# Optimization experiments

Measured on AMD Instinct MI355X. Metric: run time of the kernel, lower is better.

Reference implementation:

```python
import jax, jax.numpy as jnp
import numpy as np

MARGIN = 0.3
NEG_INF = jnp.float32(-1e30)


def setup_inputs() -> dict:
    key = jax.random.key(0)
    k1, k2 = jax.random.split(key)
    features = jax.random.normal(k1, (8192, 128), dtype=jnp.float32)
    labels = jax.random.randint(k2, (8192,), 0, 512)
    return {"features": features, "labels": labels}


def reference(features, labels):
    n = features.shape[0]
    # pairwise Euclidean distance, clamped like the torch code
    x2 = jnp.sum(features * features, axis=1, keepdims=True)          # [N,1]
    d2 = x2 + x2.T - 2.0 * (features @ features.T)                    # [N,N]
    dist = jnp.sqrt(jnp.clip(d2, 1e-8))

    same = labels[None, :] == labels[:, None]                          # [N,N]
    eye = jnp.eye(n, dtype=bool)
    pos_mask = same & ~eye                                             # positives, self excluded
    neg_mask = ~same

    # soft mining: softmax-weighted positive distance (weights ~ softmax(d))
    pos_logits = jnp.where(pos_mask, dist, NEG_INF)
    pw = jax.nn.softmax(pos_logits, axis=1)
    wp = jnp.sum(pw * jnp.where(pos_mask, dist, 0.0), axis=1)          # [N]

    # softmax-weighted negative distance (weights ~ softmax(-d))
    neg_logits = jnp.where(neg_mask, -dist, NEG_INF)
    nw = jax.nn.softmax(neg_logits, axis=1)
    wn = jnp.sum(nw * jnp.where(neg_mask, dist, 0.0), axis=1)          # [N]

    # soft margin: softplus(diff + margin)
    loss = jax.nn.softplus(wp - wn + MARGIN)

    # rows without any positive or any negative are skipped in the original
    valid = pos_mask.any(axis=1) & neg_mask.any(axis=1)
    loss = jnp.where(valid, loss, 0.0)
    denom = jnp.maximum(jnp.sum(valid.astype(jnp.float32)), 1.0)
    return jnp.sum(loss) / denom
```

## Files before the change

### kernel.cpp

```cpp
#include <hip/hip_runtime.h>
#include <hip/hip_bf16.h>


typedef __bf16 bf16x8 __attribute__((ext_vector_type(8)));
typedef float f32x4 __attribute__((ext_vector_type(4)));

#define NROWS 8192
#define DIM 128
#define JTILE 64
#define LDS_STRIDE 136
#define NLABELS 512
#define GCAP 64
#define JSPLIT 16
#define JSPAN (NROWS / JSPLIT)
#define JITERS (JSPAN / JTILE)
#define MARGIN_F 0.3f
#define AK1F 2.04027892f
#define AK1SQ 4.16273807f
#define EPS_T 2.08137e-8f
#define C2F (-43.2808512f)
#define LN2F 0.69314718f

__global__ __launch_bounds__(256) void prep_kernel(const float* __restrict__ F,
                                                   __hip_bfloat16* __restrict__ Fb,
                                                   float* __restrict__ x2,
                                                   float* __restrict__ gstat) {
    const int tid = threadIdx.x;
    const int wave = tid >> 6, lane = tid & 63;
    const int row = blockIdx.x * 4 + wave;
    float2 f = ((const float2*)(F + (size_t)row * DIM))[lane];
    f.x *= AK1F; f.y *= AK1F;
    ((__hip_bfloat162*)(Fb + (size_t)row * DIM))[lane] = __float22bfloat162_rn(f);
    float ss = f.x * f.x + f.y * f.y;
#pragma unroll
    for (int m = 32; m > 0; m >>= 1) ss += __shfl_xor(ss, m, 64);
    if (lane == 0) x2[row] = ss;
    if (blockIdx.x == 0 && tid < 4) gstat[tid] = 0.f;
}

template<bool DIAG>
__device__ __forceinline__ void tile_body(const __hip_bfloat16* __restrict__ sB,
                                          const float* __restrict__ sX2h,
                                          const bf16x8 (&a)[4],
                                          const float (&x2ih)[4],
                                          float (&nl4)[4], float (&ns4)[4],
                                          int lm, int quad, int ig0, int jbase) {
#pragma unroll
    for (int jt = 0; jt < 4; ++jt) {
        const int jl = jt * 16 + lm;
        const __hip_bfloat16* bp = sB + jl * LDS_STRIDE + quad * 8;
        const float xjh = sX2h[jl];
        f32x4 acc;
#pragma unroll
        for (int r = 0; r < 4; ++r) acc[r] = x2ih[r] + xjh;
#pragma unroll
        for (int kc = 0; kc < 4; ++kc) {
            bf16x8 b = *(const bf16x8*)(bp + kc * 32);
            acc = __builtin_amdgcn_mfma_f32_16x16x32_bf16(a[kc], b, acc, 0, 0, 0);
        }
        const int dj = jbase + jl - ig0;
#pragma unroll
        for (int r = 0; r < 4; ++r) {
            float d2h = fmaxf(-acc[r], EPS_T);
            float t = __builtin_amdgcn_sqrtf(d2h);
            float ne = __builtin_amdgcn_exp2f(-t);
            if (DIAG) ne = (dj == r) ? 0.f : ne;
            nl4[r] += ne;
            ns4[r] = fmaf(ne, t, ns4[r]);
        }
    }
}

__global__ __launch_bounds__(256, 4) void pairs_kernel(
        const __hip_bfloat16* __restrict__ Fb,
        const float* __restrict__ x2,
        const float* __restrict__ F,
        const int* __restrict__ labels,
        float2* __restrict__ partial,
        float4* __restrict__ corr) {
    __shared__ __hip_bfloat16 sB[JTILE * LDS_STRIDE];
    __shared__ float sX2[JTILE];
    __shared__ int sIdx[GCAP];
    __shared__ int sCnt;

    const int tid = threadIdx.x;
    const int bx = blockIdx.x, by = blockIdx.y;

    if (by < 4) {
        const int L = by * 128 + bx;
        if (tid == 0) sCnt = 0;
        __syncthreads();
        for (int it = 0; it < NROWS / 1024; ++it) {
            const int g = it * 1024 + tid * 4;
            int4 lv = *(const int4*)(labels + g);
#pragma unroll
            for (int k = 0; k < 4; ++k) {
                int lab = (k == 0) ? lv.x : (k == 1) ? lv.y : (k == 2) ? lv.z : lv.w;
                if (lab == L) {
                    int pos = atomicAdd(&sCnt, 1);
                    if (pos < GCAP) sIdx[pos] = g + k;
                }
            }
        }
        __syncthreads();
        const int gsz = sCnt < GCAP ? sCnt : GCAP;
        if (gsz > 0) {
            float* sAcc = (float*)sB;
            float* plA = sAcc;
            float* psA = sAcc + GCAP;
            float* nlA = sAcc + 2 * GCAP;
            float* nsA = sAcc + 3 * GCAP;
            if (tid < GCAP) { plA[tid] = 0.f; psA[tid] = 0.f; nlA[tid] = 0.f; nsA[tid] = 0.f; }
            __syncthreads();
            const int npair = gsz * gsz;
            for (int p = tid; p < npair; p += 256) {
                const int aI = p / gsz, bI = p - aI * gsz;
                if (aI == bI) continue;
                const float4* pa = (const float4*)(F + (size_t)sIdx[aI] * DIM);
                const float4* pb = (const float4*)(F + (size_t)sIdx[bI] * DIM);
                float dot = 0.f, ssa = 0.f, ssb = 0.f;
#pragma unroll 8
                for (int u = 0; u < 32; ++u) {
                    float4 va = pa[u], vb = pb[u];
                    dot = fmaf(va.x, vb.x, fmaf(va.y, vb.y, fmaf(va.z, vb.z, fmaf(va.w, vb.w, dot))));
                    ssa = fmaf(va.x, va.x, fmaf(va.y, va.y, fmaf(va.z, va.z, fmaf(va.w, va.w, ssa))));
                    ssb = fmaf(vb.x, vb.x, fmaf(vb.y, vb.y, fmaf(vb.z, vb.z, fmaf(vb.w, vb.w, ssb))));
                }
                float d2h = fmaxf((0.5f * (ssa + ssb) - dot) * AK1SQ, EPS_T);
                float t = __builtin_amdgcn_sqrtf(d2h);
                float ne = __builtin_amdgcn_exp2f(-t);
                float pe = __builtin_amdgcn_exp2f(t + C2F);
                unsafeAtomicAdd(&nlA[aI], ne);
                unsafeAtomicAdd(&nsA[aI], ne * t);
                unsafeAtomicAdd(&plA[aI], pe);
                unsafeAtomicAdd(&psA[aI], pe * t);
            }
            __syncthreads();
            if (tid < gsz)
                corr[sIdx[tid]] = make_float4(plA[tid], psA[tid], -nlA[tid], -nsA[tid]);
        }
        __syncthreads();
    }

    const int wave = tid >> 6;
    const int lane = tid & 63;
    const int quad = lane >> 4;
    const int lm = lane & 15;
    const int rbase = bx * 64 + wave * 16;

    bf16x8 a[4];
#pragma unroll
    for (int kc = 0; kc < 4; ++kc)
        a[kc] = *(const bf16x8*)(Fb + (size_t)(rbase + lm) * DIM + kc * 32 + quad * 8);

    const int ig0 = rbase + quad * 4;
    float x2ih[4];
#pragma unroll
    for (int r = 0; r < 4; ++r) x2ih[r] = -0.5f * x2[ig0 + r];

    float nl4[4] = {0,0,0,0}, ns4[4] = {0,0,0,0};

    const int j0 = by * JSPAN;
    const int djb = bx - by * JITERS;

    for (int jb = 0; jb < JITERS; ++jb) {
        const int jbase = j0 + jb * JTILE;
        __syncthreads();
#pragma unroll
        for (int s = 0; s < 4; ++s) {
            int c = tid + s * 256;
            int jr = c >> 4, ck = c & 15;
            *(bf16x8*)(sB + jr * LDS_STRIDE + ck * 8) =
                *(const bf16x8*)(Fb + (size_t)(jbase + jr) * DIM + ck * 8);
        }
        if (tid < JTILE) sX2[tid] = -0.5f * x2[jbase + tid];
        __syncthreads();

        if (jb == djb)
            tile_body<true >(sB, sX2, a, x2ih, nl4, ns4, lm, quad, ig0, jbase);
        else
            tile_body<false>(sB, sX2, a, x2ih, nl4, ns4, lm, quad, ig0, jbase);
    }

#pragma unroll
    for (int m = 1; m < 16; m <<= 1) {
#pragma unroll
        for (int r = 0; r < 4; ++r) {
            nl4[r] += __shfl_xor(nl4[r], m, 64);
            ns4[r] += __shfl_xor(ns4[r], m, 64);
        }
    }
    if (lm == 0) {
#pragma unroll
        for (int r = 0; r < 4; ++r)
            partial[(size_t)by * NROWS + ig0 + r] = make_float2(nl4[r], ns4[r]);
    }
}

__global__ __launch_bounds__(256) void finalize_kernel(const float2* __restrict__ partial,
                                                       const float4* __restrict__ corr,
                                                       float* __restrict__ gstat,
                                                       float* __restrict__ out) {
    const int row = blockIdx.x * 256 + threadIdx.x;
    float4 c = corr[row];
    float nl = c.z, ns = c.w;
#pragma unroll
    for (int s = 0; s < JSPLIT; ++s) {
        float2 p = partial[(size_t)s * NROWS + row];
        nl += p.x; ns += p.y;
    }
    float sum = 0.f, cnt = 0.f;
    if (c.x > 0.f && nl > 0.f) {
        float x = fmaf(LN2F, c.y / c.x - ns / nl, MARGIN_F);
        sum = fmaxf(x, 0.f) + log1pf(__expf(-fabsf(x)));
        cnt = 1.f;
    }
#pragma unroll
    for (int m = 32; m > 0; m >>= 1) {
        sum += __shfl_xor(sum, m, 64);
        cnt += __shfl_xor(cnt, m, 64);
    }
    __shared__ float sS[4], sC[4];
    const int wave = threadIdx.x >> 6, lane = threadIdx.x & 63;
    if (lane == 0) { sS[wave] = sum; sC[wave] = cnt; }
    __syncthreads();
    if (threadIdx.x == 0) {
        unsafeAtomicAdd(&gstat[0], sS[0] + sS[1] + sS[2] + sS[3]);
        unsafeAtomicAdd(&gstat[1], sC[0] + sC[1] + sC[2] + sC[3]);
        __threadfence();
        unsigned t = atomicAdd((unsigned*)(gstat + 2), 1u);
        if (t == (unsigned)(gridDim.x - 1)) {
            float s2 = unsafeAtomicAdd(&gstat[0], 0.f);
            float c2 = unsafeAtomicAdd(&gstat[1], 0.f);
            out[0] = s2 / fmaxf(c2, 1.f);
        }
    }
}

extern "C" void kernel_launch(void* const* d_in, const int* in_sizes, int n_in,
                              void* d_out, int out_size, void* d_ws, size_t ws_size,
                              hipStream_t stream) {
    const float* F = (const float*)d_in[0];
    const int* labels = (const int*)d_in[1];
    float* out = (float*)d_out;

    char* ws = (char*)d_ws;
    __hip_bfloat16* Fb = (__hip_bfloat16*)ws;
    size_t off = (size_t)NROWS * DIM * 2;
    float* x2 = (float*)(ws + off);    off += (size_t)NROWS * 4;
    float4* corr = (float4*)(ws + off); off += (size_t)NROWS * 16;
    float2* partial = (float2*)(ws + off);
    off += (size_t)JSPLIT * NROWS * 8;
    float* gstat = (float*)(ws + off);

    prep_kernel<<<NROWS / 4, 256, 0, stream>>>(F, Fb, x2, gstat);
    pairs_kernel<<<dim3(NROWS / 64, JSPLIT), 256, 0, stream>>>(
        Fb, x2, F, labels, partial, corr);
    finalize_kernel<<<NROWS / 256, 256, 0, stream>>>(partial, corr, gstat, out);
}
```

Measured before the change: 118.4 us.

## Spread same-label pair correction across all blocks and use bf16 features

The same-label pair correction pass used to run only in the first 4 y-rows of blocks (512 blocks, one label each), which made those blocks straggle. It now runs in all 2048 blocks, with each label split four ways by anchor index. The pairs now read the prescaled bf16 features and precomputed squared norms instead of fp32 rows, which cuts memory traffic and the redundant norm computation. In exchange, every block repeats the label scan over all 8192 labels, and the correction now uses bf16 precision, which should match the bf16 main pass more closely.

```diff
diff --git a/kernel.cpp b/kernel.cpp
--- a/kernel.cpp
+++ b/kernel.cpp
@@ -16,7 +16,6 @@
 #define JITERS (JSPAN / JTILE)
 #define MARGIN_F 0.3f
 #define AK1F 2.04027892f
-#define AK1SQ 4.16273807f
 #define EPS_T 2.08137e-8f
 #define C2F (-43.2808512f)
 #define LN2F 0.69314718f
@@ -74,7 +73,6 @@
 __global__ __launch_bounds__(256, 4) void pairs_kernel(
         const __hip_bfloat16* __restrict__ Fb,
         const float* __restrict__ x2,
-        const float* __restrict__ F,
         const int* __restrict__ labels,
         float2* __restrict__ partial,
         float4* __restrict__ corr) {
@@ -86,8 +84,9 @@
     const int tid = threadIdx.x;
     const int bx = blockIdx.x, by = blockIdx.y;
 
-    if (by < 4) {
-        const int L = by * 128 + bx;
+    {
+        const int b = by * 128 + bx;
+        const int L = b >> 2, q = b & 3;
         if (tid == 0) sCnt = 0;
         __syncthreads();
         for (int it = 0; it < NROWS / 1024; ++it) {
@@ -104,7 +103,7 @@
         }
         __syncthreads();
         const int gsz = sCnt < GCAP ? sCnt : GCAP;
-        if (gsz > 0) {
+        if (gsz > q) {
             float* sAcc = (float*)sB;
             float* plA = sAcc;
             float* psA = sAcc + GCAP;
@@ -112,21 +111,24 @@
             float* nsA = sAcc + 3 * GCAP;
             if (tid < GCAP) { plA[tid] = 0.f; psA[tid] = 0.f; nlA[tid] = 0.f; nsA[tid] = 0.f; }
             __syncthreads();
-            const int npair = gsz * gsz;
+            const int nA = (gsz - q + 3) >> 2;
+            const int npair = nA * gsz;
             for (int p = tid; p < npair; p += 256) {
-                const int aI = p / gsz, bI = p - aI * gsz;
+                const int aI = q + 4 * (p / gsz);
+                const int bI = p % gsz;
                 if (aI == bI) continue;
-                const float4* pa = (const float4*)(F + (size_t)sIdx[aI] * DIM);
-                const float4* pb = (const float4*)(F + (size_t)sIdx[bI] * DIM);
-                float dot = 0.f, ssa = 0.f, ssb = 0.f;
-#pragma unroll 8
-                for (int u = 0; u < 32; ++u) {
-                    float4 va = pa[u], vb = pb[u];
-                    dot = fmaf(va.x, vb.x, fmaf(va.y, vb.y, fmaf(va.z, vb.z, fmaf(va.w, vb.w, dot))));
-                    ssa = fmaf(va.x, va.x, fmaf(va.y, va.y, fmaf(va.z, va.z, fmaf(va.w, va.w, ssa))));
-                    ssb = fmaf(vb.x, vb.x, fmaf(vb.y, vb.y, fmaf(vb.z, vb.z, fmaf(vb.w, vb.w, ssb))));
+                const int ia = sIdx[aI], ib = sIdx[bI];
+                const bf16x8* pa = (const bf16x8*)(Fb + (size_t)ia * DIM);
+                const bf16x8* pb = (const bf16x8*)(Fb + (size_t)ib * DIM);
+                float dot = 0.f;
+#pragma unroll 4
+                for (int u = 0; u < 16; ++u) {
+                    bf16x8 va = pa[u], vb = pb[u];
+#pragma unroll
+                    for (int e = 0; e < 8; ++e)
+                        dot = fmaf((float)va[e], (float)vb[e], dot);
                 }
-                float d2h = fmaxf((0.5f * (ssa + ssb) - dot) * AK1SQ, EPS_T);
+                float d2h = fmaxf(0.5f * (x2[ia] + x2[ib]) - dot, EPS_T);
                 float t = __builtin_amdgcn_sqrtf(d2h);
                 float ne = __builtin_amdgcn_exp2f(-t);
                 float pe = __builtin_amdgcn_exp2f(t + C2F);
@@ -136,7 +138,7 @@
                 unsafeAtomicAdd(&psA[aI], pe * t);
             }
             __syncthreads();
-            if (tid < gsz)
+            if (tid < gsz && (tid & 3) == q)
                 corr[sIdx[tid]] = make_float4(plA[tid], psA[tid], -nlA[tid], -nsA[tid]);
         }
         __syncthreads();
@@ -255,6 +257,6 @@
 
     prep_kernel<<<NROWS / 4, 256, 0, stream>>>(F, Fb, x2, gstat);
     pairs_kernel<<<dim3(NROWS / 64, JSPLIT), 256, 0, stream>>>(
-        Fb, x2, F, labels, partial, corr);
+        Fb, x2, labels, partial, corr);
     finalize_kernel<<<NROWS / 256, 256, 0, stream>>>(partial, corr, gstat, out);
 }
```

New measurement: 116.4 us. About the same (-1.7%).
